# Optimization experiments

Measured on AMD Instinct MI355X. Metric: run time of the kernel, lower is better.

The kernel has to match this reference:

```python
import jax, jax.numpy as jnp
import numpy as np

B, S, H, F, E, K = 2, 2048, 1024, 2048, 8, 2  # batch, seq, hidden, ffn, experts, top_k


def setup_inputs() -> dict:
    key = jax.random.key(0)
    k1, k2, k3, k4 = jax.random.split(key, 4)
    s = lambda n: 1.0 / np.sqrt(n)
    return {
        "x": jax.random.normal(k1, (B, S, H), jnp.float32),
        "w_router": jax.random.normal(k2, (H, E), jnp.float32) * s(H),
        "w_in": jax.random.normal(k3, (E, H, 2 * F), jnp.float32) * s(H),   # GLU: 2*ffn
        "w_out": jax.random.normal(k4, (E, F, H), jnp.float32) * s(F),
        "bias": jnp.zeros((H,), jnp.float32),
    }


def reference(x, w_router, w_in, w_out, bias):
    Bq, Sq, Hq = x.shape
    T = Bq * Sq
    xf = x.reshape(T, Hq)

    # --- TopKGating ---
    logits = xf @ w_router                       # [T, E]
    top_vals, top_idx = jax.lax.top_k(logits, K)  # [T, K]
    gates = jax.nn.softmax(top_vals, axis=-1)    # softmax over selected logits

    # JetMoE-style aux loss: switch loss + 0.1 * z-loss
    probs = jax.nn.softmax(logits, axis=-1)
    p = probs.sum(0); p = p / p.sum()
    freq = jnp.sum(jax.nn.one_hot(top_idx, E, dtype=logits.dtype), axis=(0, 1))
    f = freq / freq.sum()
    lsesq = jnp.sum(jax.nn.logsumexp(logits, axis=-1) ** 2)
    loss = E * jnp.sum(p * f) + 0.1 * lsesq / T

    # --- dispatch: one row per (token, selected expert) pair, token-major ---
    eid = top_idx.reshape(-1)                    # [T*K] expert id per row
    g = gates.reshape(-1)                        # [T*K] gate per row
    tok = jnp.repeat(jnp.arange(T), K)           # [T*K] source token per row
    xr = jnp.repeat(xf, K, axis=0)               # [T*K, H]

    # --- grouped expert GEMMs (masked per-expert; math-equivalent to grouped GEMM) ---
    out_rows = jnp.zeros((T * K, Hq), x.dtype)
    for e in range(E):
        sel = (eid == e).astype(x.dtype)[:, None]
        h = (xr * sel) @ w_in[e]                 # [T*K, 2F]
        a, gv = jnp.split(h, 2, axis=-1)
        h = jax.nn.silu(a) * gv                  # GLU
        out_rows = out_rows + sel * (h @ w_out[e])

    # --- combine: scale by gates, scatter-add back to tokens ---
    out_rows = out_rows * g[:, None]
    y = jax.ops.segment_sum(out_rows, tok, num_segments=T)
    y = y.reshape(Bq, Sq, Hq) + bias
    return y, loss
```

## Files before the change

kernel.cpp:

```cpp
#include <hip/hip_runtime.h>
#include <hip/hip_bf16.h>
#include <math.h>

#define T_TOK 4096
#define HDIM  1024
#define FDIM  2048
#define EDIM  8
#define KSEL  2
#define TKROW 8192
#define N2F   4096
#define MAX_SLOTS 144

typedef __attribute__((ext_vector_type(8))) short short8;
typedef __attribute__((ext_vector_type(4))) float f32x4;

__device__ __forceinline__ unsigned short f32_to_bf16(float f) {
  unsigned int u = __float_as_uint(f);
  u += 0x7FFFu + ((u >> 16) & 1u);
  return (unsigned short)(u >> 16);
}


__global__ void conv_x_kernel(const float* __restrict__ x,
                              unsigned short* __restrict__ xb, int n) {
  int i = (blockIdx.x * blockDim.x + threadIdx.x) * 4;
  if (i < n) {
    float4 v = *(const float4*)(x + i);
    ushort4 o;
    o.x = f32_to_bf16(v.x); o.y = f32_to_bf16(v.y);
    o.z = f32_to_bf16(v.z); o.w = f32_to_bf16(v.w);
    *(ushort4*)(xb + i) = o;
  }
}

__global__ void transpose_conv_kernel(const float* __restrict__ in,
                                      unsigned short* __restrict__ out,
                                      int R, int C) {
  __shared__ float tile[64][65];
  long base = (long)blockIdx.z * (long)R * (long)C;
  int c0 = blockIdx.x * 64, r0 = blockIdx.y * 64;
  int tx = threadIdx.x & 63;
  int ty = threadIdx.x >> 6;
  #pragma unroll
  for (int j = 0; j < 64; j += 4) {
    int r = r0 + ty + j;
    tile[ty + j][tx] = in[base + (long)r * C + c0 + tx];
  }
  __syncthreads();
  #pragma unroll
  for (int j = 0; j < 64; j += 4) {
    int oc = ty + j;
    out[base + (long)(c0 + oc) * R + r0 + tx] = f32_to_bf16(tile[tx][oc]);
  }
}

__global__ void router_kernel(const float* __restrict__ x,
                              const float* __restrict__ wr,
                              int* __restrict__ eid, float* __restrict__ tgate,
                              float* __restrict__ p_sum,
                              float* __restrict__ lse2_sum,
                              int* __restrict__ counts) {
  __shared__ float s_p[EDIM];
  __shared__ float s_lse2;
  __shared__ int s_cnt[EDIM];
  if (threadIdx.x < EDIM) { s_p[threadIdx.x] = 0.f; s_cnt[threadIdx.x] = 0; }
  if (threadIdx.x == 0) s_lse2 = 0.f;
  __syncthreads();

  int wave = threadIdx.x >> 6;
  int lane = threadIdx.x & 63;

  for (int it = 0; it < 4; ++it) {
    int t = (blockIdx.x * 4 + wave) + it * 1024;
    float acc[EDIM];
    #pragma unroll
    for (int e = 0; e < EDIM; e++) acc[e] = 0.f;
    const float* xr = x + (long)t * HDIM;
    for (int h = lane; h < HDIM; h += 64) {
      float xv = xr[h];
      const float* w = wr + h * EDIM;
      #pragma unroll
      for (int e = 0; e < EDIM; e++) acc[e] += xv * w[e];
    }
    #pragma unroll
    for (int e = 0; e < EDIM; e++) {
      float v = acc[e];
      for (int off = 32; off > 0; off >>= 1) v += __shfl_down(v, off);
      acc[e] = v;
    }
    if (lane == 0) {
      float m = acc[0];
      #pragma unroll
      for (int e = 1; e < EDIM; e++) m = fmaxf(m, acc[e]);
      float ex[EDIM]; float se = 0.f;
      #pragma unroll
      for (int e = 0; e < EDIM; e++) { ex[e] = __expf(acc[e] - m); se += ex[e]; }
      float lse = m + __logf(se);
      atomicAdd(&s_lse2, lse * lse);
      float inv = 1.f / se;
      #pragma unroll
      for (int e = 0; e < EDIM; e++) atomicAdd(&s_p[e], ex[e] * inv);
      int i1 = 0;
      #pragma unroll
      for (int e = 1; e < EDIM; e++) if (acc[e] > acc[i1]) i1 = e;
      int i2 = (i1 == 0) ? 1 : 0;
      #pragma unroll
      for (int e = 0; e < EDIM; e++) if (e != i1 && acc[e] > acc[i2]) i2 = e;
      float g1 = 1.f / (1.f + __expf(acc[i2] - acc[i1]));
      eid[t * 2] = i1; eid[t * 2 + 1] = i2;
      tgate[t * 2] = g1; tgate[t * 2 + 1] = 1.f - g1;
      atomicAdd(&s_cnt[i1], 1); atomicAdd(&s_cnt[i2], 1);
    }
  }
  __syncthreads();
  if (threadIdx.x < EDIM) {
    atomicAdd(&p_sum[threadIdx.x], s_p[threadIdx.x]);
    atomicAdd(&counts[threadIdx.x], s_cnt[threadIdx.x]);
  }
  if (threadIdx.x == 0) atomicAdd(lse2_sum, s_lse2);
}

__global__ void scan_kernel(const int* __restrict__ counts,
                            int* __restrict__ offsets, int* __restrict__ slot_e,
                            int* __restrict__ slot_m0, int* __restrict__ slot_rows,
                            int* __restrict__ n_slots, int* __restrict__ cursors) {
  int off = 0, s = 0;
  for (int e = 0; e < EDIM; e++) {
    offsets[e] = off;
    cursors[e] = 0;
    int c = counts[e];
    for (int m0 = 0; m0 < c; m0 += 64) {
      slot_e[s] = e; slot_m0[s] = off + m0;
      slot_rows[s] = min(64, c - m0); s++;
    }
    off += c;
  }
  *n_slots = s;
}

__global__ void scatter_kernel(const int* __restrict__ eid,
                               const float* __restrict__ tgate,
                               const int* __restrict__ offsets,
                               int* __restrict__ cursors,
                               int* __restrict__ btok, float* __restrict__ bgate) {
  __shared__ int lcnt[EDIM];
  __shared__ int lbase[EDIM];
  int tid = threadIdx.x;
  if (tid < EDIM) lcnt[tid] = 0;
  __syncthreads();
  int t = blockIdx.x * 256 + tid;
  int e0 = eid[t * 2], e1 = eid[t * 2 + 1];
  int p0 = atomicAdd(&lcnt[e0], 1);
  int p1 = atomicAdd(&lcnt[e1], 1);
  __syncthreads();
  if (tid < EDIM) lbase[tid] = atomicAdd(&cursors[tid], lcnt[tid]);
  __syncthreads();
  int r0 = offsets[e0] + lbase[e0] + p0;
  int r1 = offsets[e1] + lbase[e1] + p1;
  btok[r0] = t; bgate[r0] = tgate[t * 2];
  btok[r1] = t; bgate[r1] = tgate[t * 2 + 1];
}

__global__ void bias_init_kernel(float* __restrict__ y,
                                 const float* __restrict__ bias, int n) {
  int i = blockIdx.x * blockDim.x + threadIdx.x;
  if (i < n) y[i] = bias[i & (HDIM - 1)];
}

__global__ __launch_bounds__(256) void gemm1_kernel(
    const unsigned short* __restrict__ xb,
    const unsigned short* __restrict__ w_inT,
    const int* __restrict__ btok,
    const int* __restrict__ slot_e, const int* __restrict__ slot_m0,
    const int* __restrict__ slot_rows, const int* __restrict__ n_slots,
    unsigned short* __restrict__ glu)
{
  int slot = blockIdx.x;
  if (slot >= *n_slots) return;
  int e = slot_e[slot], r0 = slot_m0[slot], nrows = slot_rows[slot];
  int c0 = blockIdx.y * 64;

  __shared__ unsigned short lA[64 * 40];
  __shared__ unsigned short lB[128 * 40];

  int tid = threadIdx.x;
  int arow = tid >> 2;
  int akc = tid & 3;
  int tok = (arow < nrows) ? btok[r0 + arow] : -1;
  const unsigned short* aptr =
      (tok >= 0) ? (xb + (long)tok * HDIM + akc * 8) : (const unsigned short*)0;
  const unsigned short* wbase = w_inT + (long)e * N2F * HDIM;
  const unsigned short* bptr0 = wbase + (long)(c0 + arow) * HDIM + akc * 8;
  const unsigned short* bptr1 = wbase + (long)(FDIM + c0 + arow) * HDIM + akc * 8;

  int wv = tid >> 6, lane = tid & 63;
  int lm = lane & 15, kq = lane >> 4;

  f32x4 acc[8];
  #pragma unroll
  for (int i = 0; i < 8; i++) acc[i] = (f32x4){0.f, 0.f, 0.f, 0.f};

  for (int k0 = 0; k0 < HDIM; k0 += 32) {
    if (tok >= 0) {
      *(short8*)&lA[arow * 40 + akc * 8] = *(const short8*)(aptr + k0);
    } else {
      short8 z = {0, 0, 0, 0, 0, 0, 0, 0};
      *(short8*)&lA[arow * 40 + akc * 8] = z;
    }
    *(short8*)&lB[arow * 40 + akc * 8] = *(const short8*)(bptr0 + k0);
    *(short8*)&lB[(64 + arow) * 40 + akc * 8] = *(const short8*)(bptr1 + k0);
    __syncthreads();
    short8 afrag = *(const short8*)&lA[(wv * 16 + lm) * 40 + kq * 8];
    #pragma unroll
    for (int ni = 0; ni < 8; ni++) {
      short8 bfrag = *(const short8*)&lB[(ni * 16 + lm) * 40 + kq * 8];
      acc[ni] = __builtin_amdgcn_mfma_f32_16x16x32_bf16(afrag, bfrag, acc[ni], 0, 0, 0);
    }
    __syncthreads();
  }

  #pragma unroll
  for (int r = 0; r < 4; r++) {
    int row = wv * 16 + kq * 4 + r;
    if (row < nrows) {
      #pragma unroll
      for (int ni = 0; ni < 4; ni++) {
        float a = acc[ni][r];
        float g = acc[ni + 4][r];
        float val = (a / (1.f + __expf(-a))) * g;
        glu[(long)(r0 + row) * FDIM + c0 + ni * 16 + lm] = f32_to_bf16(val);
      }
    }
  }
}

__global__ __launch_bounds__(256) void gemm2_kernel(
    const unsigned short* __restrict__ glu,
    const unsigned short* __restrict__ w_outT,
    const int* __restrict__ btok, const float* __restrict__ bgate,
    const int* __restrict__ slot_e, const int* __restrict__ slot_m0,
    const int* __restrict__ slot_rows, const int* __restrict__ n_slots,
    float* __restrict__ y)
{
  int slot = blockIdx.x;
  if (slot >= *n_slots) return;
  int e = slot_e[slot], r0 = slot_m0[slot], nrows = slot_rows[slot];
  int c0 = blockIdx.y * 64;

  __shared__ unsigned short lA[64 * 40];
  __shared__ unsigned short lB[64 * 40];

  int tid = threadIdx.x;
  int arow = tid >> 2, akc = tid & 3;
  bool avalid = (arow < nrows);
  const unsigned short* aptr = glu + (long)(r0 + arow) * FDIM + akc * 8;
  const unsigned short* bptr =
      w_outT + (long)e * HDIM * FDIM + (long)(c0 + arow) * FDIM + akc * 8;

  int wv = tid >> 6, lane = tid & 63;
  int lm = lane & 15, kq = lane >> 4;

  f32x4 acc[4];
  #pragma unroll
  for (int i = 0; i < 4; i++) acc[i] = (f32x4){0.f, 0.f, 0.f, 0.f};

  for (int k0 = 0; k0 < FDIM; k0 += 32) {
    if (avalid) {
      *(short8*)&lA[arow * 40 + akc * 8] = *(const short8*)(aptr + k0);
    } else {
      short8 z = {0, 0, 0, 0, 0, 0, 0, 0};
      *(short8*)&lA[arow * 40 + akc * 8] = z;
    }
    *(short8*)&lB[arow * 40 + akc * 8] = *(const short8*)(bptr + k0);
    __syncthreads();
    short8 afrag = *(const short8*)&lA[(wv * 16 + lm) * 40 + kq * 8];
    #pragma unroll
    for (int ni = 0; ni < 4; ni++) {
      short8 bfrag = *(const short8*)&lB[(ni * 16 + lm) * 40 + kq * 8];
      acc[ni] = __builtin_amdgcn_mfma_f32_16x16x32_bf16(afrag, bfrag, acc[ni], 0, 0, 0);
    }
    __syncthreads();
  }

  #pragma unroll
  for (int r = 0; r < 4; r++) {
    int row = wv * 16 + kq * 4 + r;
    if (row < nrows) {
      int t = btok[r0 + row];
      float g = bgate[r0 + row];
      #pragma unroll
      for (int ni = 0; ni < 4; ni++) {
        atomicAdd(&y[(long)t * HDIM + c0 + ni * 16 + lm], acc[ni][r] * g);
      }
    }
  }
}

__global__ void finalize_kernel(const float* __restrict__ p_sum,
                                const float* __restrict__ lse2,
                                const int* __restrict__ counts,
                                float* __restrict__ loss_out) {
  float P = 0.f;
  for (int e = 0; e < EDIM; e++) P += p_sum[e];
  float dot = 0.f;
  for (int e = 0; e < EDIM; e++)
    dot += (p_sum[e] / P) * ((float)counts[e] / (float)TKROW);
  *loss_out = (float)EDIM * dot + 0.1f * (*lse2) / (float)T_TOK;
}

extern "C" void kernel_launch(void* const* d_in, const int* in_sizes, int n_in,
                              void* d_out, int out_size, void* d_ws, size_t ws_size,
                              hipStream_t stream) {
  const float* x        = (const float*)d_in[0];
  const float* w_router = (const float*)d_in[1];
  const float* w_in     = (const float*)d_in[2];
  const float* w_out    = (const float*)d_in[3];
  const float* bias     = (const float*)d_in[4];
  float* y = (float*)d_out;

  char* ws = (char*)d_ws;
  size_t o = 0;
  auto alloc = [&](size_t bytes) { size_t r = o; o = (o + bytes + 255) & ~(size_t)255; return r; };
  size_t o_meta    = alloc(256);
  size_t o_offsets = alloc(EDIM * 4);
  size_t o_slot_e  = alloc(MAX_SLOTS * 4);
  size_t o_slot_m0 = alloc(MAX_SLOTS * 4);
  size_t o_slot_nr = alloc(MAX_SLOTS * 4);
  size_t o_eid     = alloc((size_t)T_TOK * 2 * 4);
  size_t o_tgate   = alloc((size_t)T_TOK * 2 * 4);
  size_t o_btok    = alloc((size_t)TKROW * 4);
  size_t o_bgate   = alloc((size_t)TKROW * 4);
  size_t o_xb      = alloc((size_t)T_TOK * HDIM * 2);
  size_t o_winT    = alloc((size_t)EDIM * N2F * HDIM * 2);
  size_t o_woutT   = alloc((size_t)EDIM * HDIM * FDIM * 2);
  size_t o_glu     = alloc((size_t)TKROW * FDIM * 2);
  (void)ws_size;

  float* p_sum   = (float*)(ws + o_meta);
  float* lse2    = (float*)(ws + o_meta + 32);
  int*   counts  = (int*)(ws + o_meta + 64);
  int*   cursors = (int*)(ws + o_meta + 96);
  int*   n_slots = (int*)(ws + o_meta + 128);
  int*   offsets = (int*)(ws + o_offsets);
  int*   slot_e  = (int*)(ws + o_slot_e);
  int*   slot_m0 = (int*)(ws + o_slot_m0);
  int*   slot_nr = (int*)(ws + o_slot_nr);
  int*   eid     = (int*)(ws + o_eid);
  float* tgate   = (float*)(ws + o_tgate);
  int*   btok    = (int*)(ws + o_btok);
  float* bgate   = (float*)(ws + o_bgate);
  unsigned short* xb    = (unsigned short*)(ws + o_xb);
  unsigned short* winT  = (unsigned short*)(ws + o_winT);
  unsigned short* woutT = (unsigned short*)(ws + o_woutT);
  unsigned short* glu   = (unsigned short*)(ws + o_glu);

  hipMemsetAsync(ws, 0, 256, stream);

  conv_x_kernel<<<dim3((T_TOK * HDIM) / 1024), dim3(256), 0, stream>>>(
      x, xb, T_TOK * HDIM);
  transpose_conv_kernel<<<dim3(N2F / 64, HDIM / 64, EDIM), dim3(256), 0, stream>>>(
      w_in, winT, HDIM, N2F);
  transpose_conv_kernel<<<dim3(HDIM / 64, FDIM / 64, EDIM), dim3(256), 0, stream>>>(
      w_out, woutT, FDIM, HDIM);

  router_kernel<<<dim3(256), dim3(256), 0, stream>>>(
      x, w_router, eid, tgate, p_sum, lse2, counts);
  scan_kernel<<<dim3(1), dim3(1), 0, stream>>>(
      counts, offsets, slot_e, slot_m0, slot_nr, n_slots, cursors);
  scatter_kernel<<<dim3(T_TOK / 256), dim3(256), 0, stream>>>(
      eid, tgate, offsets, cursors, btok, bgate);

  bias_init_kernel<<<dim3((T_TOK * HDIM) / 256), dim3(256), 0, stream>>>(
      y, bias, T_TOK * HDIM);

  gemm1_kernel<<<dim3(136, FDIM / 64), dim3(256), 0, stream>>>(
      xb, winT, btok, slot_e, slot_m0, slot_nr, n_slots, glu);
  gemm2_kernel<<<dim3(136, HDIM / 64), dim3(256), 0, stream>>>(
      glu, woutT, btok, bgate, slot_e, slot_m0, slot_nr, n_slots, y);

  finalize_kernel<<<dim3(1), dim3(1), 0, stream>>>(
      p_sum, lse2, counts, y + (size_t)T_TOK * HDIM);
}
```

Before: 618.1 us.

## Use 128-row expert tiles with direct global-to-LDS loads in MoE GEMMs

```diff
diff --git a/kernel.cpp b/kernel.cpp
--- a/kernel.cpp
+++ b/kernel.cpp
@@ -6,10 +6,9 @@
 #define HDIM  1024
 #define FDIM  2048
 #define EDIM  8
-#define KSEL  2
 #define TKROW 8192
 #define N2F   4096
-#define MAX_SLOTS 144
+#define MAX_SLOTS 80
 
 typedef __attribute__((ext_vector_type(8))) short short8;
 typedef __attribute__((ext_vector_type(4))) float f32x4;
@@ -18,6 +17,12 @@
   unsigned int u = __float_as_uint(f);
   u += 0x7FFFu + ((u >> 16) & 1u);
   return (unsigned short)(u >> 16);
+}
+
+__device__ __forceinline__ void gload_lds16(const void* g, void* l) {
+  __builtin_amdgcn_global_load_lds(
+      (const __attribute__((address_space(1))) unsigned int*)g,
+      (__attribute__((address_space(3))) unsigned int*)l, 16, 0, 0);
 }
 
 
@@ -39,18 +44,21 @@
   __shared__ float tile[64][65];
   long base = (long)blockIdx.z * (long)R * (long)C;
   int c0 = blockIdx.x * 64, r0 = blockIdx.y * 64;
-  int tx = threadIdx.x & 63;
-  int ty = threadIdx.x >> 6;
+  int tx = (threadIdx.x & 15) * 4;
+  int ty = threadIdx.x >> 4;
+  #pragma unroll
+  for (int j = 0; j < 64; j += 16) {
+    int r = r0 + ty + j;
+    float4 v = *(const float4*)&in[base + (long)r * C + c0 + tx];
+    tile[ty + j][tx] = v.x; tile[ty + j][tx + 1] = v.y;
+    tile[ty + j][tx + 2] = v.z; tile[ty + j][tx + 3] = v.w;
+  }
+  __syncthreads();
+  int tx2 = threadIdx.x & 63, ty2 = threadIdx.x >> 6;
   #pragma unroll
   for (int j = 0; j < 64; j += 4) {
-    int r = r0 + ty + j;
-    tile[ty + j][tx] = in[base + (long)r * C + c0 + tx];
-  }
-  __syncthreads();
-  #pragma unroll
-  for (int j = 0; j < 64; j += 4) {
-    int oc = ty + j;
-    out[base + (long)(c0 + oc) * R + r0 + tx] = f32_to_bf16(tile[tx][oc]);
+    int oc = ty2 + j;
+    out[base + (long)(c0 + oc) * R + r0 + tx2] = f32_to_bf16(tile[tx2][oc]);
   }
 }
 
@@ -129,9 +137,9 @@
     offsets[e] = off;
     cursors[e] = 0;
     int c = counts[e];
-    for (int m0 = 0; m0 < c; m0 += 64) {
+    for (int m0 = 0; m0 < c; m0 += 128) {
       slot_e[s] = e; slot_m0[s] = off + m0;
-      slot_rows[s] = min(64, c - m0); s++;
+      slot_rows[s] = min(128, c - m0); s++;
     }
     off += c;
   }
@@ -180,55 +188,72 @@
   int e = slot_e[slot], r0 = slot_m0[slot], nrows = slot_rows[slot];
   int c0 = blockIdx.y * 64;
 
-  __shared__ unsigned short lA[64 * 40];
-  __shared__ unsigned short lB[128 * 40];
+  __shared__ unsigned short lA[4096];
+  __shared__ unsigned short lB[4096];
 
   int tid = threadIdx.x;
-  int arow = tid >> 2;
-  int akc = tid & 3;
-  int tok = (arow < nrows) ? btok[r0 + arow] : -1;
-  const unsigned short* aptr =
-      (tok >= 0) ? (xb + (long)tok * HDIM + akc * 8) : (const unsigned short*)0;
-  const unsigned short* wbase = w_inT + (long)e * N2F * HDIM;
-  const unsigned short* bptr0 = wbase + (long)(c0 + arow) * HDIM + akc * 8;
-  const unsigned short* bptr1 = wbase + (long)(FDIM + c0 + arow) * HDIM + akc * 8;
+  int sr = tid & 127;
+  int sc0 = tid >> 7;
+  int tokA = (sr < nrows) ? btok[r0 + sr] : btok[r0];
+  const unsigned short* agp = xb + (long)tokA * HDIM + sc0 * 8;
+  int brow = (sr < 64) ? (c0 + sr) : (FDIM + c0 + (sr - 64));
+  const unsigned short* bgp = w_inT + (long)e * N2F * HDIM + (long)brow * HDIM + sc0 * 8;
+
+  char* lAb = (char*)lA;
+  char* lBb = (char*)lB;
+  int d0 = tid * 16;
 
   int wv = tid >> 6, lane = tid & 63;
+  int wm = (wv & 1) * 64;
+  int wn = (wv >> 1);
   int lm = lane & 15, kq = lane >> 4;
 
-  f32x4 acc[8];
-  #pragma unroll
-  for (int i = 0; i < 8; i++) acc[i] = (f32x4){0.f, 0.f, 0.f, 0.f};
+  const char* pA = (const char*)lA + kq * 2048 + (wm + lm) * 16;
+  const char* pB = (const char*)lB + kq * 2048 + (wn * 32 + lm) * 16;
+
+  f32x4 acc[4][4];
+  #pragma unroll
+  for (int i = 0; i < 4; i++)
+    #pragma unroll
+    for (int j = 0; j < 4; j++) acc[i][j] = (f32x4){0.f, 0.f, 0.f, 0.f};
 
   for (int k0 = 0; k0 < HDIM; k0 += 32) {
-    if (tok >= 0) {
-      *(short8*)&lA[arow * 40 + akc * 8] = *(const short8*)(aptr + k0);
-    } else {
-      short8 z = {0, 0, 0, 0, 0, 0, 0, 0};
-      *(short8*)&lA[arow * 40 + akc * 8] = z;
-    }
-    *(short8*)&lB[arow * 40 + akc * 8] = *(const short8*)(bptr0 + k0);
-    *(short8*)&lB[(64 + arow) * 40 + akc * 8] = *(const short8*)(bptr1 + k0);
+    gload_lds16(agp,      lAb + d0);
+    gload_lds16(agp + 16, lAb + d0 + 4096);
+    gload_lds16(bgp,      lBb + d0);
+    gload_lds16(bgp + 16, lBb + d0 + 4096);
+    agp += 32; bgp += 32;
     __syncthreads();
-    short8 afrag = *(const short8*)&lA[(wv * 16 + lm) * 40 + kq * 8];
-    #pragma unroll
-    for (int ni = 0; ni < 8; ni++) {
-      short8 bfrag = *(const short8*)&lB[(ni * 16 + lm) * 40 + kq * 8];
-      acc[ni] = __builtin_amdgcn_mfma_f32_16x16x32_bf16(afrag, bfrag, acc[ni], 0, 0, 0);
-    }
+
+    short8 af[4], bf[4];
+    #pragma unroll
+    for (int mi = 0; mi < 4; mi++) af[mi] = *(const short8*)(pA + mi * 256);
+    bf[0] = *(const short8*)(pB);
+    bf[1] = *(const short8*)(pB + 256);
+    bf[2] = *(const short8*)(pB + 1024);
+    bf[3] = *(const short8*)(pB + 1024 + 256);
+    #pragma unroll
+    for (int mi = 0; mi < 4; mi++)
+      #pragma unroll
+      for (int ni = 0; ni < 4; ni++)
+        acc[mi][ni] = __builtin_amdgcn_mfma_f32_16x16x32_bf16(af[mi], bf[ni], acc[mi][ni], 0, 0, 0);
     __syncthreads();
   }
 
   #pragma unroll
-  for (int r = 0; r < 4; r++) {
-    int row = wv * 16 + kq * 4 + r;
-    if (row < nrows) {
-      #pragma unroll
-      for (int ni = 0; ni < 4; ni++) {
-        float a = acc[ni][r];
-        float g = acc[ni + 4][r];
-        float val = (a / (1.f + __expf(-a))) * g;
-        glu[(long)(r0 + row) * FDIM + c0 + ni * 16 + lm] = f32_to_bf16(val);
+  for (int mi = 0; mi < 4; mi++) {
+    #pragma unroll
+    for (int rr = 0; rr < 4; rr++) {
+      int row = wm + mi * 16 + kq * 4 + rr;
+      if (row < nrows) {
+        #pragma unroll
+        for (int ni = 0; ni < 2; ni++) {
+          float a = acc[mi][ni][rr];
+          float g = acc[mi][ni + 2][rr];
+          float val = (a / (1.f + __expf(-a))) * g;
+          int col = c0 + wn * 32 + ni * 16 + lm;
+          glu[(long)(r0 + row) * FDIM + col] = f32_to_bf16(val);
+        }
       }
     }
   }
@@ -245,52 +270,70 @@
   int slot = blockIdx.x;
   if (slot >= *n_slots) return;
   int e = slot_e[slot], r0 = slot_m0[slot], nrows = slot_rows[slot];
-  int c0 = blockIdx.y * 64;
-
-  __shared__ unsigned short lA[64 * 40];
-  __shared__ unsigned short lB[64 * 40];
+  int c0 = blockIdx.y * 128;
+
+  __shared__ unsigned short lA[4096];
+  __shared__ unsigned short lB[4096];
 
   int tid = threadIdx.x;
-  int arow = tid >> 2, akc = tid & 3;
-  bool avalid = (arow < nrows);
-  const unsigned short* aptr = glu + (long)(r0 + arow) * FDIM + akc * 8;
-  const unsigned short* bptr =
-      w_outT + (long)e * HDIM * FDIM + (long)(c0 + arow) * FDIM + akc * 8;
+  int sr = tid & 127;
+  int sc0 = tid >> 7;
+  const unsigned short* agp = glu + (long)(r0 + sr) * FDIM + sc0 * 8;
+  const unsigned short* bgp =
+      w_outT + (long)e * HDIM * FDIM + (long)(c0 + sr) * FDIM + sc0 * 8;
+
+  char* lAb = (char*)lA;
+  char* lBb = (char*)lB;
+  int d0 = tid * 16;
 
   int wv = tid >> 6, lane = tid & 63;
+  int wm = (wv & 1) * 64;
+  int wn = (wv >> 1) * 64;
   int lm = lane & 15, kq = lane >> 4;
 
-  f32x4 acc[4];
-  #pragma unroll
-  for (int i = 0; i < 4; i++) acc[i] = (f32x4){0.f, 0.f, 0.f, 0.f};
+  const char* pA = (const char*)lA + kq * 2048 + (wm + lm) * 16;
+  const char* pB = (const char*)lB + kq * 2048 + (wn + lm) * 16;
+
+  f32x4 acc[4][4];
+  #pragma unroll
+  for (int i = 0; i < 4; i++)
+    #pragma unroll
+    for (int j = 0; j < 4; j++) acc[i][j] = (f32x4){0.f, 0.f, 0.f, 0.f};
 
   for (int k0 = 0; k0 < FDIM; k0 += 32) {
-    if (avalid) {
-      *(short8*)&lA[arow * 40 + akc * 8] = *(const short8*)(aptr + k0);
-    } else {
-      short8 z = {0, 0, 0, 0, 0, 0, 0, 0};
-      *(short8*)&lA[arow * 40 + akc * 8] = z;
-    }
-    *(short8*)&lB[arow * 40 + akc * 8] = *(const short8*)(bptr + k0);
+    gload_lds16(agp,      lAb + d0);
+    gload_lds16(agp + 16, lAb + d0 + 4096);
+    gload_lds16(bgp,      lBb + d0);
+    gload_lds16(bgp + 16, lBb + d0 + 4096);
+    agp += 32; bgp += 32;
     __syncthreads();
-    short8 afrag = *(const short8*)&lA[(wv * 16 + lm) * 40 + kq * 8];
-    #pragma unroll
-    for (int ni = 0; ni < 4; ni++) {
-      short8 bfrag = *(const short8*)&lB[(ni * 16 + lm) * 40 + kq * 8];
-      acc[ni] = __builtin_amdgcn_mfma_f32_16x16x32_bf16(afrag, bfrag, acc[ni], 0, 0, 0);
-    }
+
+    short8 af[4], bf[4];
+    #pragma unroll
+    for (int mi = 0; mi < 4; mi++) af[mi] = *(const short8*)(pA + mi * 256);
+    #pragma unroll
+    for (int ni = 0; ni < 4; ni++) bf[ni] = *(const short8*)(pB + ni * 256);
+    #pragma unroll
+    for (int mi = 0; mi < 4; mi++)
+      #pragma unroll
+      for (int ni = 0; ni < 4; ni++)
+        acc[mi][ni] = __builtin_amdgcn_mfma_f32_16x16x32_bf16(af[mi], bf[ni], acc[mi][ni], 0, 0, 0);
     __syncthreads();
   }
 
   #pragma unroll
-  for (int r = 0; r < 4; r++) {
-    int row = wv * 16 + kq * 4 + r;
-    if (row < nrows) {
-      int t = btok[r0 + row];
-      float g = bgate[r0 + row];
-      #pragma unroll
-      for (int ni = 0; ni < 4; ni++) {
-        atomicAdd(&y[(long)t * HDIM + c0 + ni * 16 + lm], acc[ni][r] * g);
+  for (int mi = 0; mi < 4; mi++) {
+    #pragma unroll
+    for (int rr = 0; rr < 4; rr++) {
+      int row = wm + mi * 16 + kq * 4 + rr;
+      if (row < nrows) {
+        int t = btok[r0 + row];
+        float g = bgate[r0 + row];
+        #pragma unroll
+        for (int ni = 0; ni < 4; ni++) {
+          int col = c0 + wn + ni * 16 + lm;
+          atomicAdd(&y[(long)t * HDIM + col], acc[mi][ni][rr] * g);
+        }
       }
     }
   }
@@ -328,12 +371,12 @@
   size_t o_slot_nr = alloc(MAX_SLOTS * 4);
   size_t o_eid     = alloc((size_t)T_TOK * 2 * 4);
   size_t o_tgate   = alloc((size_t)T_TOK * 2 * 4);
-  size_t o_btok    = alloc((size_t)TKROW * 4);
-  size_t o_bgate   = alloc((size_t)TKROW * 4);
+  size_t o_btok    = alloc((size_t)(TKROW + 128) * 4);
+  size_t o_bgate   = alloc((size_t)(TKROW + 128) * 4);
   size_t o_xb      = alloc((size_t)T_TOK * HDIM * 2);
   size_t o_winT    = alloc((size_t)EDIM * N2F * HDIM * 2);
   size_t o_woutT   = alloc((size_t)EDIM * HDIM * FDIM * 2);
-  size_t o_glu     = alloc((size_t)TKROW * FDIM * 2);
+  size_t o_glu     = alloc((size_t)(TKROW + 128) * FDIM * 2);
   (void)ws_size;
 
   float* p_sum   = (float*)(ws + o_meta);
@@ -373,9 +416,9 @@
   bias_init_kernel<<<dim3((T_TOK * HDIM) / 256), dim3(256), 0, stream>>>(
       y, bias, T_TOK * HDIM);
 
-  gemm1_kernel<<<dim3(136, FDIM / 64), dim3(256), 0, stream>>>(
+  gemm1_kernel<<<dim3(MAX_SLOTS, FDIM / 64), dim3(256), 0, stream>>>(
       xb, winT, btok, slot_e, slot_m0, slot_nr, n_slots, glu);
-  gemm2_kernel<<<dim3(136, HDIM / 64), dim3(256), 0, stream>>>(
+  gemm2_kernel<<<dim3(MAX_SLOTS, HDIM / 128), dim3(256), 0, stream>>>(
       glu, woutT, btok, bgate, slot_e, slot_m0, slot_nr, n_slots, y);
 
   finalize_kernel<<<dim3(1), dim3(1), 0, stream>>>(
```

After: 657.1 us. +6.3%, slower.
